# Optimization experiments

Measured on AMD Instinct MI355X. Metric: run time of the kernel, lower is better.

Reference implementation:

```python
import jax, jax.numpy as jnp
import numpy as np

EMB_DIM = 128
HEAD_SIZE = 16  # embDim // numHea = 128 // 8


def setup_inputs() -> dict:
    key = jax.random.key(0)
    k1, k2, k3, k4 = jax.random.split(key, 4)
    B, T = 8, 2048
    inpEmb = jax.random.normal(k1, (B, T, EMB_DIM), dtype=jnp.float32)
    # nn.Linear(embDim, heaSiz, bias=False) weights, stored transposed so y = x @ W
    Wq = jax.random.normal(k2, (EMB_DIM, HEAD_SIZE), dtype=jnp.float32) / np.sqrt(EMB_DIM)
    Wk = jax.random.normal(k3, (EMB_DIM, HEAD_SIZE), dtype=jnp.float32) / np.sqrt(EMB_DIM)
    Wv = jax.random.normal(k4, (EMB_DIM, HEAD_SIZE), dtype=jnp.float32) / np.sqrt(EMB_DIM)
    return {"inpEmb": inpEmb, "Wq": Wq, "Wk": Wk, "Wv": Wv}


def reference(inpEmb, Wq, Wk, Wv):
    # q,k,v: [B, T, H]
    q = inpEmb @ Wq
    k = inpEmb @ Wk
    v = inpEmb @ Wv
    scale = HEAD_SIZE ** -0.5
    # scores: [B, T, T]
    scores = jnp.einsum('bqh,bkh->bqk', q, k) * scale
    T = inpEmb.shape[1]
    causal = jnp.tril(jnp.ones((T, T), dtype=bool))
    scores = jnp.where(causal, scores, -jnp.inf)
    weights = jax.nn.softmax(scores, axis=-1)
    # dropout treated as identity (eval mode) for deterministic reference
    return jnp.einsum('bqk,bkh->bqh', weights, v)
```

## Files before the change

kernel.cpp:

```cpp
#include <hip/hip_runtime.h>
#include <hip/hip_bf16.h>

#define T_SEQ 2048
#define EMB   128
#define H     16
#define BATCH 8
#define VSTR  2064
#define QSCALE 0.360673760222241f

#define EXP2F(x) __builtin_amdgcn_exp2f(x)

typedef short short8_t __attribute__((ext_vector_type(8)));
typedef float f32x4    __attribute__((ext_vector_type(4)));

__device__ __forceinline__ unsigned short f2bf(float f) {
    __hip_bfloat16 h = __float2bfloat16(f);
    return *reinterpret_cast<unsigned short*>(&h);
}

__global__ __launch_bounds__(192) void qkv_kernel(
    const float* __restrict__ x,
    const float* __restrict__ Wq,
    const float* __restrict__ Wk,
    const float* __restrict__ Wv,
    unsigned short* __restrict__ Qbf,
    unsigned short* __restrict__ Kbf,
    unsigned short* __restrict__ Vt)
{
    const int tid  = threadIdx.x;
    const int wv   = tid >> 6;
    const int lane = tid & 63;
    const int q    = lane >> 4;
    const int n    = lane & 15;
    const int r0   = blockIdx.x * 16;

    const float* Wm = (wv == 0) ? Wq : (wv == 1) ? Wk : Wv;
    const float* xr = x + (size_t)(r0 + n) * EMB;

    f32x4 a = {0.f, 0.f, 0.f, 0.f};
#pragma unroll
    for (int t = 0; t < 4; ++t) {
        const int k0 = t * 32 + q * 8;
        float4 xa = *reinterpret_cast<const float4*>(xr + k0);
        float4 xb = *reinterpret_cast<const float4*>(xr + k0 + 4);
        union { unsigned short s[8]; short8_t v; } xf;
        xf.s[0]=f2bf(xa.x); xf.s[1]=f2bf(xa.y); xf.s[2]=f2bf(xa.z); xf.s[3]=f2bf(xa.w);
        xf.s[4]=f2bf(xb.x); xf.s[5]=f2bf(xb.y); xf.s[6]=f2bf(xb.z); xf.s[7]=f2bf(xb.w);
        union { unsigned short s[8]; short8_t v; } wf;
#pragma unroll
        for (int j = 0; j < 8; ++j)
            wf.s[j] = f2bf(Wm[(size_t)(k0 + j) * H + n]);
        a = __builtin_amdgcn_mfma_f32_16x16x32_bf16(xf.v, wf.v, a, 0, 0, 0);
    }

    const int grow = r0 + q * 4;
    if (wv == 0) {
#pragma unroll
        for (int r = 0; r < 4; ++r)
            Qbf[(size_t)(grow + r) * H + n] = f2bf(a[r] * QSCALE);
    } else if (wv == 1) {
#pragma unroll
        for (int r = 0; r < 4; ++r)
            Kbf[(size_t)(grow + r) * H + n] = f2bf(a[r]);
    } else {
        const int b   = grow >> 11;
        const int ib0 = grow & 2047;
        union { unsigned short s[4]; unsigned long long u; } vp;
        vp.s[0]=f2bf(a[0]); vp.s[1]=f2bf(a[1]); vp.s[2]=f2bf(a[2]); vp.s[3]=f2bf(a[3]);
        *reinterpret_cast<unsigned long long*>(
            Vt + ((size_t)b * H + n) * VSTR + ib0) = vp.u;
    }
}

__global__ __launch_bounds__(512, 4) void attn_fused(
    const unsigned short* __restrict__ Qbf,
    const unsigned short* __restrict__ Kbf,
    const unsigned short* __restrict__ Vt,
    float* __restrict__ out)
{
    __shared__ union {
        unsigned int P[8][16][68];
        struct {
            float A[8][16][20];
            float L[8][16];
        } comb;
    } sh;

    const int qt = (T_SEQ / 16 - 1) - blockIdx.x;
    const int b  = blockIdx.y;
    const int i0 = qt << 4;
    const int nc = (qt >> 3) + 1;

    const int tid  = threadIdx.x;
    const int wv   = tid >> 6;
    const int lane = tid & 63;
    const int q    = lane >> 4;
    const int n    = lane & 15;
    const int irow = i0 + n;

    const unsigned short* Qp = Qbf + (size_t)b * T_SEQ * H;
    const unsigned short* Kp = Kbf + (size_t)b * T_SEQ * H;
    const unsigned short* vrow = Vt + (size_t)b * H * VSTR + (size_t)n * VSTR;

    short8_t qf = {0,0,0,0,0,0,0,0};
    if (q < 2)
        qf = *reinterpret_cast<const short8_t*>(Qp + (size_t)irow * H + q * 8);

    f32x4 acc = {0.f, 0.f, 0.f, 0.f};
    float l = 0.f;

    int c = wv;
    short8_t kcur[8];
#pragma unroll
    for (int s = 0; s < 8; ++s) kcur[s] = (short8_t){0,0,0,0,0,0,0,0};
    if (c < nc && q < 2) {
        const int j0 = c << 7;
#pragma unroll
        for (int s = 0; s < 8; ++s)
            kcur[s] = *reinterpret_cast<const short8_t*>(
                          Kp + (size_t)(j0 + s * 16 + n) * H + q * 8);
    }

    for (; c < nc; c += 8) {
        const int j0 = c << 7;

        f32x4 S[8];
#pragma unroll
        for (int s = 0; s < 8; ++s) {
            f32x4 z = {0.f, 0.f, 0.f, 0.f};
            S[s] = __builtin_amdgcn_mfma_f32_16x16x32_bf16(kcur[s], qf, z, 0, 0, 0);
        }
        const int c2 = c + 8;
        if (c2 < nc && q < 2) {
            const int j2 = c2 << 7;
#pragma unroll
            for (int s = 0; s < 8; ++s)
                kcur[s] = *reinterpret_cast<const short8_t*>(
                              Kp + (size_t)(j2 + s * 16 + n) * H + q * 8);
        }
        short8_t vf[4];
#pragma unroll
        for (int h = 0; h < 4; ++h)
            vf[h] = *reinterpret_cast<const short8_t*>(vrow + j0 + h * 32 + q * 8);

        if (j0 + 127 > i0) {
#pragma unroll
            for (int s = 0; s < 8; ++s) {
                const int kb = j0 + s * 16 + q * 4;
#pragma unroll
                for (int rr = 0; rr < 4; ++rr)
                    S[s][rr] = (kb + rr <= irow) ? S[s][rr] : -1e30f;
            }
        }

        float lc = 0.f;
#pragma unroll
        for (int s = 0; s < 8; ++s) {
            float e0 = EXP2F(S[s][0]);
            float e1 = EXP2F(S[s][1]);
            float e2 = EXP2F(S[s][2]);
            float e3 = EXP2F(S[s][3]);
            lc += (e0 + e1) + (e2 + e3);
            unsigned int b0 = __builtin_bit_cast(unsigned int, e0);
            unsigned int b1 = __builtin_bit_cast(unsigned int, e1);
            unsigned int b2 = __builtin_bit_cast(unsigned int, e2);
            unsigned int b3 = __builtin_bit_cast(unsigned int, e3);
            unsigned long long pw =
                (unsigned long long)((b1 & 0xffff0000u) | (b0 >> 16)) |
                ((unsigned long long)((b3 & 0xffff0000u) | (b2 >> 16)) << 32);
            *reinterpret_cast<unsigned long long*>(&sh.P[wv][n][8 * s + 2 * q]) = pw;
        }
        l += lc;

#pragma unroll
        for (int h = 0; h < 4; ++h) {
            uint4 p4 = *reinterpret_cast<const uint4*>(&sh.P[wv][n][16 * h + 4 * q]);
            union { uint4 u; short8_t v; } pu; pu.u = p4;
            acc = __builtin_amdgcn_mfma_f32_16x16x32_bf16(vf[h], pu.v, acc, 0, 0, 0);
        }
    }

    l += __shfl_xor(l, 16);
    l += __shfl_xor(l, 32);

    __syncthreads();

    *reinterpret_cast<float4*>(&sh.comb.A[wv][n][4 * q]) =
        (float4){acc[0], acc[1], acc[2], acc[3]};
    if (q == 0) sh.comb.L[wv][n] = l;
    __syncthreads();

    if (tid < 256) {
        const int row = tid >> 4;
        const int d   = tid & 15;
        float L = 0.f, O = 0.f;
#pragma unroll
        for (int w = 0; w < 8; ++w) {
            L += sh.comb.L[w][row];
            O += sh.comb.A[w][row][d];
        }
        out[((size_t)b * T_SEQ + i0 + row) * H + d] = O / L;
    }
}

extern "C" void kernel_launch(void* const* d_in, const int* in_sizes, int n_in,
                              void* d_out, int out_size, void* d_ws, size_t ws_size,
                              hipStream_t stream)
{
    const float* x  = (const float*)d_in[0];
    const float* Wq = (const float*)d_in[1];
    const float* Wk = (const float*)d_in[2];
    const float* Wv = (const float*)d_in[3];
    float* out = (float*)d_out;

    const size_t NE = (size_t)BATCH * T_SEQ * H;
    unsigned short* Qbf = (unsigned short*)d_ws;
    unsigned short* Kbf = Qbf + NE;
    unsigned short* Vt  = Kbf + NE;

    qkv_kernel<<<BATCH * T_SEQ / 16, 192, 0, stream>>>(
        x, Wq, Wk, Wv, Qbf, Kbf, Vt);
    attn_fused<<<dim3(T_SEQ / 16, BATCH), 512, 0, stream>>>(Qbf, Kbf, Vt, out);
}
```

Before: 76.11 us.

## Pair heavy and light query tiles per block, split key chunks over four waves

The attention kernel now handles two query tiles per block: the four waves of one half process tile `bid`, and the other four process the mirrored tile `1023-bid`. Each tile's key chunks are split across 4 waves instead of 8. Pairing short and long causal rows evens out per-block work and halves the block count. The QKV projection kernel also processes two 16-row groups per 384-thread block. The cost is that each tile gets half the intra-tile parallelism, so the longest tiles run longer chains per wave.

```diff
diff --git a/kernel.cpp b/kernel.cpp
--- a/kernel.cpp
+++ b/kernel.cpp
@@ -18,7 +18,7 @@
     return *reinterpret_cast<unsigned short*>(&h);
 }
 
-__global__ __launch_bounds__(192) void qkv_kernel(
+__global__ __launch_bounds__(384) void qkv_kernel(
     const float* __restrict__ x,
     const float* __restrict__ Wq,
     const float* __restrict__ Wk,
@@ -28,13 +28,15 @@
     unsigned short* __restrict__ Vt)
 {
     const int tid  = threadIdx.x;
-    const int wv   = tid >> 6;
+    const int w    = tid >> 6;
+    const int grp  = (w >= 3) ? 1 : 0;
+    const int m    = w - 3 * grp;
     const int lane = tid & 63;
     const int q    = lane >> 4;
     const int n    = lane & 15;
-    const int r0   = blockIdx.x * 16;
-
-    const float* Wm = (wv == 0) ? Wq : (wv == 1) ? Wk : Wv;
+    const int r0   = (blockIdx.x * 2 + grp) * 16;
+
+    const float* Wm = (m == 0) ? Wq : (m == 1) ? Wk : Wv;
     const float* xr = x + (size_t)(r0 + n) * EMB;
 
     f32x4 a = {0.f, 0.f, 0.f, 0.f};
@@ -54,11 +56,11 @@
     }
 
     const int grow = r0 + q * 4;
-    if (wv == 0) {
+    if (m == 0) {
 #pragma unroll
         for (int r = 0; r < 4; ++r)
             Qbf[(size_t)(grow + r) * H + n] = f2bf(a[r] * QSCALE);
-    } else if (wv == 1) {
+    } else if (m == 1) {
 #pragma unroll
         for (int r = 0; r < 4; ++r)
             Kbf[(size_t)(grow + r) * H + n] = f2bf(a[r]);
@@ -86,16 +88,19 @@
         } comb;
     } sh;
 
-    const int qt = (T_SEQ / 16 - 1) - blockIdx.x;
-    const int b  = blockIdx.y;
-    const int i0 = qt << 4;
-    const int nc = (qt >> 3) + 1;
-
     const int tid  = threadIdx.x;
     const int wv   = tid >> 6;
+    const int tl   = wv >> 2;
+    const int sp   = wv & 3;
     const int lane = tid & 63;
     const int q    = lane >> 4;
     const int n    = lane & 15;
+    const int bid  = blockIdx.x;
+    const int gt   = tl ? (1023 - bid) : bid;
+    const int b    = gt & 7;
+    const int qt   = gt >> 3;
+    const int i0   = qt << 4;
+    const int nc   = (qt >> 3) + 1;
     const int irow = i0 + n;
 
     const unsigned short* Qp = Qbf + (size_t)b * T_SEQ * H;
@@ -109,7 +114,7 @@
     f32x4 acc = {0.f, 0.f, 0.f, 0.f};
     float l = 0.f;
 
-    int c = wv;
+    int c = sp;
     short8_t kcur[8];
 #pragma unroll
     for (int s = 0; s < 8; ++s) kcur[s] = (short8_t){0,0,0,0,0,0,0,0};
@@ -121,7 +126,7 @@
                           Kp + (size_t)(j0 + s * 16 + n) * H + q * 8);
     }
 
-    for (; c < nc; c += 8) {
+    for (; c < nc; c += 4) {
         const int j0 = c << 7;
 
         f32x4 S[8];
@@ -130,7 +135,7 @@
             f32x4 z = {0.f, 0.f, 0.f, 0.f};
             S[s] = __builtin_amdgcn_mfma_f32_16x16x32_bf16(kcur[s], qf, z, 0, 0, 0);
         }
-        const int c2 = c + 8;
+        const int c2 = c + 4;
         if (c2 < nc && q < 2) {
             const int j2 = c2 << 7;
 #pragma unroll
@@ -190,16 +195,20 @@
     if (q == 0) sh.comb.L[wv][n] = l;
     __syncthreads();
 
-    if (tid < 256) {
-        const int row = tid >> 4;
-        const int d   = tid & 15;
+    {
+        const int tile = tid >> 8;
+        const int row  = (tid >> 4) & 15;
+        const int d    = tid & 15;
+        const int gt2  = tile ? (1023 - bid) : bid;
+        const int b2   = gt2 & 7;
+        const int i02  = (gt2 >> 3) << 4;
         float L = 0.f, O = 0.f;
 #pragma unroll
-        for (int w = 0; w < 8; ++w) {
-            L += sh.comb.L[w][row];
-            O += sh.comb.A[w][row][d];
-        }
-        out[((size_t)b * T_SEQ + i0 + row) * H + d] = O / L;
+        for (int w2 = 0; w2 < 4; ++w2) {
+            L += sh.comb.L[4 * tile + w2][row];
+            O += sh.comb.A[4 * tile + w2][row][d];
+        }
+        out[((size_t)b2 * T_SEQ + i02 + row) * H + d] = O / L;
     }
 }
 
@@ -218,7 +227,7 @@
     unsigned short* Kbf = Qbf + NE;
     unsigned short* Vt  = Kbf + NE;
 
-    qkv_kernel<<<BATCH * T_SEQ / 16, 192, 0, stream>>>(
+    qkv_kernel<<<BATCH * T_SEQ / 32, 384, 0, stream>>>(
         x, Wq, Wk, Wv, Qbf, Kbf, Vt);
-    attn_fused<<<dim3(T_SEQ / 16, BATCH), 512, 0, stream>>>(Qbf, Kbf, Vt, out);
-}
+    attn_fused<<<T_SEQ / 16 * BATCH / 2, 512, 0, stream>>>(Qbf, Kbf, Vt, out);
+}
```

After: 73.98 us. 2.8% less time.
